# Kernel tuning notes

Hardware: AMD Instinct MI355X
Metric: run time of the kernel (lower is better)

Reference implementation:

```python
import jax, jax.numpy as jnp
import numpy as np

B, T, D = 64, 512, 1024
H0, H1 = 1024, 1024

def setup_inputs() -> dict:
    key = jax.random.key(0)
    k1, k2, k3 = jax.random.split(key, 3)
    # scale weights ~ 1/sqrt(fan_in) so tanh doesn't saturate
    s0 = 1.0 / np.sqrt(H0 + D)
    s1 = 1.0 / np.sqrt(H1 + H0)
    return {
        "x": jax.random.normal(k1, (B, T, D), dtype=jnp.float32),
        "W0": jax.random.normal(k2, (H0 + D, H0), dtype=jnp.float32) * s0,
        "b0": jnp.zeros((H0,), dtype=jnp.float32),
        "W1": jax.random.normal(k3, (H1 + H0, H1), dtype=jnp.float32) * s1,
        "b1": jnp.zeros((H1,), dtype=jnp.float32),
    }

def reference(x, W0, b0, W1, b1):
    batch = x.shape[0]
    h0_init = jnp.zeros((batch, W0.shape[1]), dtype=x.dtype)
    h1_init = jnp.zeros((batch, W1.shape[1]), dtype=x.dtype)

    def step(carry, xt):
        h0, h1 = carry
        # layer 0: concat(prev hidden, input) -> dense -> tanh
        h0 = jnp.tanh(jnp.concatenate([h0, xt], axis=-1) @ W0 + b0)
        # layer 1 consumes layer 0 output
        h1 = jnp.tanh(jnp.concatenate([h1, h0], axis=-1) @ W1 + b1)
        return (h0, h1), h1

    xs = jnp.swapaxes(x, 0, 1)  # [T, B, D] time-major for scan
    (h0_f, h1_f), ys = jax.lax.scan(step, (h0_init, h1_init), xs)
    outputs = jnp.swapaxes(ys, 0, 1)  # [B, T, H1]
    final_state = jnp.concatenate([h0_f, h1_f], axis=-1)  # [B, H0+H1]
    return outputs, final_state
```

## Files before the change

kernel.cpp:

```cpp
#include <hip/hip_runtime.h>
#include <cmath>


typedef unsigned short u16;
typedef unsigned int   u32;
typedef unsigned long long u64;
typedef __bf16 bf16x8 __attribute__((ext_vector_type(8)));
typedef u16    u16x8  __attribute__((ext_vector_type(8)));
typedef u16    u16x4  __attribute__((ext_vector_type(4)));
typedef float  f32x4  __attribute__((ext_vector_type(4)));

constexpr int BB = 64;
constexpr int TT = 512;
constexpr size_t SLOT   = (size_t)64 * 1024;
constexpr size_t SLAB_B = SLOT * 2;

constexpr size_t OFF_W0T = 262144;
constexpr size_t OFF_W1T = OFF_W0T + (size_t)1024 * 2048 * 2;
constexpr size_t OFF_R   = OFF_W1T + (size_t)1024 * 2048 * 2;

constexpr int LDS_REQ = 159744;

__device__ inline u16 f2bf(float f) { return __builtin_bit_cast(u16, (__bf16)f); }
__device__ inline float bf2f(u16 v) { return (float)__builtin_bit_cast(__bf16, v); }
__device__ inline float fast_tanh(float x) {
  x = fminf(15.f, fmaxf(-15.f, x));
  float e = __expf(2.f * x);
  return (e - 1.f) * __builtin_amdgcn_rcpf(e + 1.f);
}

__global__ void zero_flags(unsigned* f) {
  int i = blockIdx.x * 256 + threadIdx.x;
  if (i < 3 * 512 * 32) f[i] = 0;
}

__global__ void transpose_w(const float* __restrict__ W0,
                            const float* __restrict__ W1,
                            u16* __restrict__ wt_base) {
  __shared__ float tile[64][65];
  int bi  = blockIdx.x;
  int mat = bi >> 9;
  int t   = bi & 511;
  int tk = t & 31, tn = t >> 5;
  const float* W = mat ? W1 : W0;
  u16* Wt = wt_base + (size_t)mat * 1024 * 2048;
  int K0 = tk * 64, N0 = tn * 64;
  int tid = threadIdx.x;
  {
    int c4 = (tid & 15) * 4;
    int r  = tid >> 4;
    for (int i = 0; i < 4; ++i) {
      int kl = r + i * 16;
      float4 v = *(const float4*)(W + (size_t)(K0 + kl) * 1024 + N0 + c4);
      tile[kl][c4 + 0] = v.x; tile[kl][c4 + 1] = v.y;
      tile[kl][c4 + 2] = v.z; tile[kl][c4 + 3] = v.w;
    }
  }
  __syncthreads();
  {
    int nl = tid >> 3;
    int kc = (tid & 7) * 8;
    for (int pass = 0; pass < 2; ++pass) {
      int n = nl + pass * 32;
      u16x8 o;
      #pragma unroll
      for (int z = 0; z < 8; ++z) o[z] = f2bf(tile[kc + z][n]);
      *(u16x8*)(Wt + (size_t)(N0 + n) * 2048 + K0 + kc) = o;
    }
  }
}

__global__ void xconv(const float* __restrict__ x, u16* __restrict__ xb) {
  int bi = blockIdx.x;
  int b = bi >> 9, t = bi & 511;
  const float* src = x + ((size_t)b * TT + t) * 1024;
  u16* dst = xb + ((size_t)t * BB + b) * 1024;
  int i = threadIdx.x * 4;
  float4 v = *(const float4*)(src + i);
  u16x4 o; o[0] = f2bf(v.x); o[1] = f2bf(v.y); o[2] = f2bf(v.z); o[3] = f2bf(v.w);
  *(u16x4*)(dst + i) = o;
}

__device__ inline void poll1(unsigned* p) {
  while (__hip_atomic_load(p, __ATOMIC_RELAXED, __HIP_MEMORY_SCOPE_SYSTEM) == 0u)
    __builtin_amdgcn_s_sleep(1);
}

template<bool COHA>
__device__ inline void load_a8(const u16* Abase, size_t aoff, bf16x8* a) {
  const u16* ap = Abase + aoff;
  #pragma unroll
  for (int ks = 0; ks < 8; ++ks) {
    if constexpr (COHA) {
      u64 lo = __hip_atomic_load((u64*)(ap + ks * 32),     __ATOMIC_RELAXED, __HIP_MEMORY_SCOPE_SYSTEM);
      u64 hi = __hip_atomic_load((u64*)(ap + ks * 32 + 4), __ATOMIC_RELAXED, __HIP_MEMORY_SCOPE_SYSTEM);
      union { u64 q2[2]; bf16x8 v; } un; un.q2[0] = lo; un.q2[1] = hi;
      a[ks] = un.v;
    } else {
      a[ks] = __builtin_bit_cast(bf16x8, *(const u16x8*)(ap + ks * 32));
    }
  }
}

__device__ inline void fma8(const bf16x8* a, const u16* bp,
                            int gbase, int n15, f32x4& acc0, f32x4& acc1) {
  #pragma unroll
  for (int ks = 0; ks < 8; ++ks) {
    int g = (gbase + 4 * ks) ^ n15;
    bf16x8 b0 = __builtin_bit_cast(bf16x8, *(const u16x8*)(bp + g * 8));
    bf16x8 b1 = __builtin_bit_cast(bf16x8, *(const u16x8*)(bp + 16 * 1024 + g * 8));
    acc0 = __builtin_amdgcn_mfma_f32_16x16x32_bf16(a[ks], b0, acc0, 0, 0, 0);
    acc1 = __builtin_amdgcn_mfma_f32_16x16x32_bf16(a[ks], b1, acc1, 0, 0, 0);
  }
}

template<bool COH>
__global__ void __launch_bounds__(1024, 1)
rnn_seq(const float* __restrict__ x, const float* __restrict__ b0v,
        const float* __restrict__ b1v, float* __restrict__ out,
        unsigned* __restrict__ flags, const u16* __restrict__ W0t,
        const u16* __restrict__ W1t, u16* __restrict__ h0r,
        u16* __restrict__ h1r, u16* __restrict__ ur,
        const u16* __restrict__ xb, int use_xb) {
  constexpr int RMASK = COH ? 15 : 511;
  constexpr int UMASK = COH ? 31 : 511;
  constexpr int RING = 16, URING = 32;
  extern __shared__ u16 lds[];
  unsigned* fl_h0 = flags;
  unsigned* fl_h1 = flags + 512 * 32;
  unsigned* fl_u  = flags + 2 * 512 * 32;

  int wg = blockIdx.x, tid = threadIdx.x;
  int grp = wg >> 5, j = wg & 31;
  int n0 = j * 32;
  int lane = tid & 63, wave = tid >> 6;
  int rb = wave & 3;
  int ksl = wave >> 2;
  int n15 = lane & 15, q = lane >> 4;
  int r0 = rb * 16;

  u16*   wlds = lds;
  float* scr  = (float*)((char*)lds + ((grp == 1) ? 131072 : 65536));
  u16*   hch  = (u16*)((char*)scr + 24576);

  {
    const u16* Wt = (grp == 1) ? W1t : W0t;
    int nh = (grp == 1) ? 2 : 1;
    for (int h = 0; h < nh; ++h) {
      int kb = (grp == 1) ? h * 1024 : (grp == 2 ? 1024 : 0);
      for (int idx = tid; idx < 32 * 128; idx += 1024) {
        int n = idx >> 7, g = idx & 127;
        u16x8 v = *(const u16x8*)(Wt + (size_t)(n0 + n) * 2048 + kb + g * 8);
        *(u16x8*)(wlds + h * 32768 + n * 1024 + ((g ^ (n & 15)) * 8)) = v;
      }
    }
  }
  __syncthreads();

  const size_t aoff = (size_t)(r0 + n15) * 1024 + ksl * 256 + q * 8;
  const int gbase = 32 * ksl + q;
  const u16* bp0 = wlds + n15 * 1024;
  const u16* bp1 = wlds + 32768 + n15 * 1024;

  const int slice = wave >> 2;
  const int half  = slice >> 1;
  const int ksl2  = slice & 1;
  const size_t aoffS = (size_t)(r0 + n15) * 1024 + ksl2 * 512 + q * 8;
  const int gbaseS = 64 * ksl2 + q;
  const u16* bpH = half ? bp0 : bp1;

  const int sb  = tid >> 4;
  const int scc = (tid & 15) * 2;
  const int rbT = sb >> 4, rr = sb & 15;

  float bia = 0.f, bib = 0.f;
  if (grp == 1) { bia = b1v[n0 + n15]; bib = b1v[n0 + n15 + 16]; }
  float2 b2x = {0.f, 0.f};
  if (grp == 2) b2x = *(const float2*)&b0v[n0 + scc];

  auto scr_write = [&](int s, const f32x4& a0, const f32x4& a1) {
    int base = ((rb * 3 + s - 1) * 2) * 256 + (q * 4) * 16 + n15;
    #pragma unroll
    for (int i = 0; i < 4; ++i) scr[base + i * 16] = a0[i];
    #pragma unroll
    for (int i = 0; i < 4; ++i) scr[base + 256 + i * 16] = a1[i];
  };
  auto scr_sum = [&](f32x4& a0, f32x4& a1) {
    #pragma unroll
    for (int s = 0; s < 3; ++s) {
      int base = ((rb * 3 + s) * 2) * 256 + (q * 4) * 16 + n15;
      #pragma unroll
      for (int i = 0; i < 4; ++i) a0[i] += scr[base + i * 16];
      #pragma unroll
      for (int i = 0; i < 4; ++i) a1[i] += scr[base + 256 + i * 16];
    }
  };

  auto scr_put = [&](const f32x4& a0, const f32x4& a1) {
    int base = rb * 2048 + ksl * 512 + (q * 4) * 16 + n15;
    #pragma unroll
    for (int i = 0; i < 4; ++i) scr[base + i * 16] = a0[i];
    #pragma unroll
    for (int i = 0; i < 4; ++i) scr[base + 256 + i * 16] = a1[i];
  };
  auto col_sum = [&](int c2) -> float {
    int base = rbT * 2048 + (c2 >> 4) * 256 + rr * 16 + (c2 & 15);
    return (scr[base] + scr[base + 512]) + (scr[base + 1024] + scr[base + 1536]);
  };

  const size_t FIN = (size_t)BB * TT * 1024;

  if (grp == 0) {
    for (int t = 0; t < TT; ++t) {
      if (tid < 32)      { if (t > 0)            poll1(&fl_h0[(t - 1) * 32 + tid]); }
      else if (tid < 64) {                       poll1(&fl_u [t * 32 + (tid - 32)]); }
      else if (tid < 96) { if (COH && t >= RING) poll1(&fl_h1[(t - RING) * 32 + (tid - 64)]); }
      __syncthreads();
      bf16x8 a[8];
      if (t > 0) load_a8<COH>(h0r + (size_t)((t - 1) & RMASK) * SLOT, aoff, a);
      u32 uval;
      {
        const u32* up = (const u32*)(ur + (size_t)(t & UMASK) * SLOT + sb * 1024 + n0 + scc);
        uval = COH ? __hip_atomic_load((u32*)up, __ATOMIC_RELAXED, __HIP_MEMORY_SCOPE_SYSTEM)
                   : *up;
      }
      f32x4 acc0 = {0.f, 0.f, 0.f, 0.f}, acc1 = acc0;
      if (t > 0) fma8(a, bp0, gbase, n15, acc0, acc1);
      scr_put(acc0, acc1);
      __syncthreads();
      float v0 = fast_tanh(col_sum(scc)     + bf2f((u16)(uval & 0xffffu)));
      float v1 = fast_tanh(col_sum(scc + 1) + bf2f((u16)(uval >> 16)));
      u32 pv = (u32)f2bf(v0) | ((u32)f2bf(v1) << 16);
      __hip_atomic_store((u32*)(h0r + (size_t)(t & RMASK) * SLOT + sb * 1024 + n0 + scc),
                         pv, __ATOMIC_RELAXED, __HIP_MEMORY_SCOPE_SYSTEM);
      __syncthreads();
      if (tid == 0)
        __hip_atomic_store(&fl_h0[t * 32 + j], 1u, __ATOMIC_RELAXED, __HIP_MEMORY_SCOPE_SYSTEM);
      if (t == TT - 1) {
        float2 o; o.x = v0; o.y = v1;
        *(float2*)&out[FIN + (size_t)sb * 2048 + n0 + scc] = o;
      }
    }
  } else if (grp == 1) {
    for (int t = 0; t < TT; ++t) {
      if (tid < 32)      { poll1(&fl_h0[t * 32 + tid]); }
      else if (tid < 64) { if (t > 0) poll1(&fl_h1[(t - 1) * 32 + (tid - 32)]); }
      __syncthreads();
      f32x4 acc0 = {0.f, 0.f, 0.f, 0.f}, acc1 = acc0;
      if (half == 0) {
        bf16x8 a[16];
        const u16* s0 = h0r + (size_t)(t & RMASK) * SLOT;
        load_a8<COH>(s0, aoffS, a);
        load_a8<COH>(s0, aoffS + 256, a + 8);
        fma8(a,     bpH, gbaseS,      n15, acc0, acc1);
        fma8(a + 8, bpH, gbaseS + 32, n15, acc0, acc1);
      } else if (t > 0) {
        bf16x8 a[16];
        const u16* s1 = h1r + (size_t)((t - 1) & RMASK) * SLOT;
        load_a8<COH>(s1, aoffS, a);
        load_a8<COH>(s1, aoffS + 256, a + 8);
        fma8(a,     bpH, gbaseS,      n15, acc0, acc1);
        fma8(a + 8, bpH, gbaseS + 32, n15, acc0, acc1);
      }
      if (slice > 0) scr_write(slice, acc0, acc1);
      __syncthreads();
      if (slice == 0) {
        scr_sum(acc0, acc1);
        #pragma unroll
        for (int i = 0; i < 4; ++i) {
          int b = r0 + q * 4 + i;
          hch[b * 32 + n15]      = f2bf(fast_tanh(acc0[i] + bia));
          hch[b * 32 + n15 + 16] = f2bf(fast_tanh(acc1[i] + bib));
        }
      }
      __syncthreads();
      u32 pv = ((u32*)hch)[tid];
      __hip_atomic_store((u32*)(h1r + (size_t)(t & RMASK) * SLOT + sb * 1024 + n0 + scc),
                         pv, __ATOMIC_RELAXED, __HIP_MEMORY_SCOPE_SYSTEM);
      __syncthreads();
      if (tid == 0)
        __hip_atomic_store(&fl_h1[t * 32 + j], 1u, __ATOMIC_RELAXED, __HIP_MEMORY_SCOPE_SYSTEM);
      {
        float2 o; o.x = bf2f((u16)(pv & 0xffffu)); o.y = bf2f((u16)(pv >> 16));
        __builtin_nontemporal_store(o.x, &out[((size_t)sb * TT + t) * 1024 + n0 + scc]);
        __builtin_nontemporal_store(o.y, &out[((size_t)sb * TT + t) * 1024 + n0 + scc + 1]);
        if (t == TT - 1)
          *(float2*)&out[FIN + (size_t)sb * 2048 + 1024 + n0 + scc] = o;
      }
    }
  } else {
    for (int t = 0; t < TT; ++t) {
      if (COH && t >= URING) {
        if (tid < 32) poll1(&fl_h0[(t - URING) * 32 + tid]);
      }
      __syncthreads();
      bf16x8 a[8];
      if (use_xb) {
        load_a8<false>(xb + (size_t)t * SLOT, aoff, a);
      } else {
        const float* Ap = x + ((size_t)(r0 + n15) * TT + t) * 1024 + ksl * 256 + q * 8;
        float4 f[16];
        #pragma unroll
        for (int ks = 0; ks < 8; ++ks) {
          f[2 * ks]     = *(const float4*)(Ap + ks * 32);
          f[2 * ks + 1] = *(const float4*)(Ap + ks * 32 + 4);
        }
        #pragma unroll
        for (int ks = 0; ks < 8; ++ks) {
          bf16x8 tv;
          tv[0] = (__bf16)f[2*ks].x;   tv[1] = (__bf16)f[2*ks].y;
          tv[2] = (__bf16)f[2*ks].z;   tv[3] = (__bf16)f[2*ks].w;
          tv[4] = (__bf16)f[2*ks+1].x; tv[5] = (__bf16)f[2*ks+1].y;
          tv[6] = (__bf16)f[2*ks+1].z; tv[7] = (__bf16)f[2*ks+1].w;
          a[ks] = tv;
        }
      }
      f32x4 acc0 = {0.f, 0.f, 0.f, 0.f}, acc1 = acc0;
      fma8(a, bp0, gbase, n15, acc0, acc1);
      scr_put(acc0, acc1);
      __syncthreads();
      float v0 = col_sum(scc)     + b2x.x;
      float v1 = col_sum(scc + 1) + b2x.y;
      u32 pv = (u32)f2bf(v0) | ((u32)f2bf(v1) << 16);
      __hip_atomic_store((u32*)(ur + (size_t)(t & UMASK) * SLOT + sb * 1024 + n0 + scc),
                         pv, __ATOMIC_RELAXED, __HIP_MEMORY_SCOPE_SYSTEM);
      __syncthreads();
      if (tid == 0)
        __hip_atomic_store(&fl_u[t * 32 + j], 1u, __ATOMIC_RELAXED, __HIP_MEMORY_SCOPE_SYSTEM);
    }
  }
}

extern "C" void kernel_launch(void* const* d_in, const int* in_sizes, int n_in,
                              void* d_out, int out_size, void* d_ws, size_t ws_size,
                              hipStream_t stream) {
  const float* x  = (const float*)d_in[0];
  const float* W0 = (const float*)d_in[1];
  const float* b0 = (const float*)d_in[2];
  const float* W1 = (const float*)d_in[3];
  const float* b1 = (const float*)d_in[4];
  float* out = (float*)d_out;
  unsigned char* ws = (unsigned char*)d_ws;

  const size_t WS_PLAIN = OFF_R + 4ull * 512 * SLAB_B;
  bool plain = ws_size >= WS_PLAIN;
  size_t nslot  = plain ? 512 : 16;
  size_t nuslot = plain ? 512 : 32;
  size_t o_h0 = OFF_R;
  size_t o_h1 = o_h0 + nslot  * SLAB_B;
  size_t o_u  = o_h1 + nslot  * SLAB_B;
  size_t o_xb = o_u  + nuslot * SLAB_B;
  int use_xb = (plain || ws_size >= o_xb + (size_t)TT * SLAB_B) ? 1 : 0;

  unsigned* flags = (unsigned*)ws;
  const u16* W0t = (const u16*)(ws + OFF_W0T);
  const u16* W1t = (const u16*)(ws + OFF_W1T);
  u16* h0r = (u16*)(ws + o_h0);
  u16* h1r = (u16*)(ws + o_h1);
  u16* ur  = (u16*)(ws + o_u);
  u16* xb  = (u16*)(ws + o_xb);

  zero_flags<<<192, 256, 0, stream>>>(flags);
  transpose_w<<<1024, 256, 0, stream>>>(W0, W1, (u16*)(ws + OFF_W0T));
  if (use_xb) xconv<<<32768, 256, 0, stream>>>(x, xb);

  (void)hipFuncSetAttribute((const void*)rnn_seq<false>,
                            hipFuncAttributeMaxDynamicSharedMemorySize, LDS_REQ);
  (void)hipFuncSetAttribute((const void*)rnn_seq<true>,
                            hipFuncAttributeMaxDynamicSharedMemorySize, LDS_REQ);

  void* args[12];
  args[0]  = (void*)&x;    args[1]  = (void*)&b0;   args[2]  = (void*)&b1;
  args[3]  = (void*)&out;  args[4]  = (void*)&flags;
  args[5]  = (void*)&W0t;  args[6]  = (void*)&W1t;
  args[7]  = (void*)&h0r;  args[8]  = (void*)&h1r;  args[9]  = (void*)&ur;
  args[10] = (void*)&xb;   args[11] = (void*)&use_xb;
  hipLaunchCooperativeKernel(plain ? (void*)rnn_seq<false> : (void*)rnn_seq<true>,
                             dim3(96), dim3(1024), args, LDS_REQ, stream);
}
```

Before: 4.873 ms.

## Replace flag polling with sentinel-poisoned data polling in non-ring path

```diff
diff --git a/kernel.cpp b/kernel.cpp
--- a/kernel.cpp
+++ b/kernel.cpp
@@ -10,6 +10,9 @@
 typedef u16    u16x4  __attribute__((ext_vector_type(4)));
 typedef float  f32x4  __attribute__((ext_vector_type(4)));
 
+#define SCOPE_SYS __HIP_MEMORY_SCOPE_SYSTEM
+constexpr u32 SENT32 = 0x7FC07FC0u;
+
 constexpr int BB = 64;
 constexpr int TT = 512;
 constexpr size_t SLOT   = (size_t)64 * 1024;
@@ -32,6 +35,13 @@
 __global__ void zero_flags(unsigned* f) {
   int i = blockIdx.x * 256 + threadIdx.x;
   if (i < 3 * 512 * 32) f[i] = 0;
+}
+
+__global__ void poison(u32* p, size_t n4) {
+  size_t i = (size_t)blockIdx.x * 256 + threadIdx.x;
+  uint4 q = {SENT32, SENT32, SENT32, SENT32};
+  for (; i < n4; i += (size_t)gridDim.x * 256)
+    ((uint4*)p)[i] = q;
 }
 
 __global__ void transpose_w(const float* __restrict__ W0,
@@ -82,8 +92,39 @@
 }
 
 __device__ inline void poll1(unsigned* p) {
-  while (__hip_atomic_load(p, __ATOMIC_RELAXED, __HIP_MEMORY_SCOPE_SYSTEM) == 0u)
+  while (__hip_atomic_load(p, __ATOMIC_RELAXED, SCOPE_SYS) == 0u)
     __builtin_amdgcn_s_sleep(1);
+}
+
+template<int NF>
+__device__ inline void poll_frags(const u16* base, size_t off, bf16x8* a) {
+  const u16* p = base + off;
+  u64 lo[NF], hi[NF];
+  #pragma unroll
+  for (int i = 0; i < NF; ++i) {
+    lo[i] = __hip_atomic_load((const u64*)(p + i * 32),     __ATOMIC_RELAXED, SCOPE_SYS);
+    hi[i] = __hip_atomic_load((const u64*)(p + i * 32 + 4), __ATOMIC_RELAXED, SCOPE_SYS);
+  }
+  for (;;) {
+    u32 bad = 0;
+    #pragma unroll
+    for (int i = 0; i < NF; ++i) {
+      bad |= ((u32)lo[i] == SENT32) | ((u32)(lo[i] >> 32) == SENT32)
+           | ((u32)hi[i] == SENT32) | ((u32)(hi[i] >> 32) == SENT32);
+    }
+    if (!bad) break;
+    __builtin_amdgcn_s_sleep(1);
+    #pragma unroll
+    for (int i = 0; i < NF; ++i) {
+      lo[i] = __hip_atomic_load((const u64*)(p + i * 32),     __ATOMIC_RELAXED, SCOPE_SYS);
+      hi[i] = __hip_atomic_load((const u64*)(p + i * 32 + 4), __ATOMIC_RELAXED, SCOPE_SYS);
+    }
+  }
+  #pragma unroll
+  for (int i = 0; i < NF; ++i) {
+    union { u64 q2[2]; bf16x8 v; } un; un.q2[0] = lo[i]; un.q2[1] = hi[i];
+    a[i] = un.v;
+  }
 }
 
 template<bool COHA>
@@ -92,8 +133,8 @@
   #pragma unroll
   for (int ks = 0; ks < 8; ++ks) {
     if constexpr (COHA) {
-      u64 lo = __hip_atomic_load((u64*)(ap + ks * 32),     __ATOMIC_RELAXED, __HIP_MEMORY_SCOPE_SYSTEM);
-      u64 hi = __hip_atomic_load((u64*)(ap + ks * 32 + 4), __ATOMIC_RELAXED, __HIP_MEMORY_SCOPE_SYSTEM);
+      u64 lo = __hip_atomic_load((u64*)(ap + ks * 32),     __ATOMIC_RELAXED, SCOPE_SYS);
+      u64 hi = __hip_atomic_load((u64*)(ap + ks * 32 + 4), __ATOMIC_RELAXED, SCOPE_SYS);
       union { u64 q2[2]; bf16x8 v; } un; un.q2[0] = lo; un.q2[1] = hi;
       a[ks] = un.v;
     } else {
@@ -211,122 +252,226 @@
   const size_t FIN = (size_t)BB * TT * 1024;
 
   if (grp == 0) {
-    for (int t = 0; t < TT; ++t) {
-      if (tid < 32)      { if (t > 0)            poll1(&fl_h0[(t - 1) * 32 + tid]); }
-      else if (tid < 64) {                       poll1(&fl_u [t * 32 + (tid - 32)]); }
-      else if (tid < 96) { if (COH && t >= RING) poll1(&fl_h1[(t - RING) * 32 + (tid - 64)]); }
-      __syncthreads();
-      bf16x8 a[8];
-      if (t > 0) load_a8<COH>(h0r + (size_t)((t - 1) & RMASK) * SLOT, aoff, a);
-      u32 uval;
-      {
-        const u32* up = (const u32*)(ur + (size_t)(t & UMASK) * SLOT + sb * 1024 + n0 + scc);
-        uval = COH ? __hip_atomic_load((u32*)up, __ATOMIC_RELAXED, __HIP_MEMORY_SCOPE_SYSTEM)
-                   : *up;
-      }
-      f32x4 acc0 = {0.f, 0.f, 0.f, 0.f}, acc1 = acc0;
-      if (t > 0) fma8(a, bp0, gbase, n15, acc0, acc1);
-      scr_put(acc0, acc1);
-      __syncthreads();
-      float v0 = fast_tanh(col_sum(scc)     + bf2f((u16)(uval & 0xffffu)));
-      float v1 = fast_tanh(col_sum(scc + 1) + bf2f((u16)(uval >> 16)));
-      u32 pv = (u32)f2bf(v0) | ((u32)f2bf(v1) << 16);
-      __hip_atomic_store((u32*)(h0r + (size_t)(t & RMASK) * SLOT + sb * 1024 + n0 + scc),
-                         pv, __ATOMIC_RELAXED, __HIP_MEMORY_SCOPE_SYSTEM);
-      __syncthreads();
-      if (tid == 0)
-        __hip_atomic_store(&fl_h0[t * 32 + j], 1u, __ATOMIC_RELAXED, __HIP_MEMORY_SCOPE_SYSTEM);
-      if (t == TT - 1) {
-        float2 o; o.x = v0; o.y = v1;
-        *(float2*)&out[FIN + (size_t)sb * 2048 + n0 + scc] = o;
+    if constexpr (!COH) {
+      for (int t = 0; t < TT; ++t) {
+        const u32* up = (const u32*)(ur + (size_t)t * SLOT + sb * 1024 + n0 + scc);
+        u32 uval = __hip_atomic_load(up, __ATOMIC_RELAXED, SCOPE_SYS);
+        f32x4 acc0 = {0.f, 0.f, 0.f, 0.f}, acc1 = acc0;
+        if (t > 0) {
+          bf16x8 a[8];
+          poll_frags<8>(h0r + (size_t)(t - 1) * SLOT, aoff, a);
+          fma8(a, bp0, gbase, n15, acc0, acc1);
+        }
+        scr_put(acc0, acc1);
+        __syncthreads();
+        float s0 = col_sum(scc), s1 = col_sum(scc + 1);
+        while (uval == SENT32) {
+          __builtin_amdgcn_s_sleep(1);
+          uval = __hip_atomic_load(up, __ATOMIC_RELAXED, SCOPE_SYS);
+        }
+        float v0 = fast_tanh(s0 + bf2f((u16)(uval & 0xffffu)));
+        float v1 = fast_tanh(s1 + bf2f((u16)(uval >> 16)));
+        u32 pv = (u32)f2bf(v0) | ((u32)f2bf(v1) << 16);
+        __syncthreads();
+        __hip_atomic_store((u32*)(h0r + (size_t)t * SLOT + sb * 1024 + n0 + scc),
+                           pv, __ATOMIC_RELAXED, SCOPE_SYS);
+        if (t == TT - 1) {
+          float2 o; o.x = v0; o.y = v1;
+          *(float2*)&out[FIN + (size_t)sb * 2048 + n0 + scc] = o;
+        }
+      }
+    } else {
+      for (int t = 0; t < TT; ++t) {
+        if (tid < 32)      { if (t > 0)            poll1(&fl_h0[(t - 1) * 32 + tid]); }
+        else if (tid < 64) {                       poll1(&fl_u [t * 32 + (tid - 32)]); }
+        else if (tid < 96) { if (t >= RING)        poll1(&fl_h1[(t - RING) * 32 + (tid - 64)]); }
+        __syncthreads();
+        bf16x8 a[8];
+        if (t > 0) load_a8<true>(h0r + (size_t)((t - 1) & RMASK) * SLOT, aoff, a);
+        u32 uval;
+        {
+          const u32* up = (const u32*)(ur + (size_t)(t & UMASK) * SLOT + sb * 1024 + n0 + scc);
+          uval = __hip_atomic_load((u32*)up, __ATOMIC_RELAXED, SCOPE_SYS);
+        }
+        f32x4 acc0 = {0.f, 0.f, 0.f, 0.f}, acc1 = acc0;
+        if (t > 0) fma8(a, bp0, gbase, n15, acc0, acc1);
+        scr_put(acc0, acc1);
+        __syncthreads();
+        float v0 = fast_tanh(col_sum(scc)     + bf2f((u16)(uval & 0xffffu)));
+        float v1 = fast_tanh(col_sum(scc + 1) + bf2f((u16)(uval >> 16)));
+        u32 pv = (u32)f2bf(v0) | ((u32)f2bf(v1) << 16);
+        __hip_atomic_store((u32*)(h0r + (size_t)(t & RMASK) * SLOT + sb * 1024 + n0 + scc),
+                           pv, __ATOMIC_RELAXED, SCOPE_SYS);
+        __syncthreads();
+        if (tid == 0)
+          __hip_atomic_store(&fl_h0[t * 32 + j], 1u, __ATOMIC_RELAXED, SCOPE_SYS);
+        if (t == TT - 1) {
+          float2 o; o.x = v0; o.y = v1;
+          *(float2*)&out[FIN + (size_t)sb * 2048 + n0 + scc] = o;
+        }
       }
     }
   } else if (grp == 1) {
-    for (int t = 0; t < TT; ++t) {
-      if (tid < 32)      { poll1(&fl_h0[t * 32 + tid]); }
-      else if (tid < 64) { if (t > 0) poll1(&fl_h1[(t - 1) * 32 + (tid - 32)]); }
-      __syncthreads();
-      f32x4 acc0 = {0.f, 0.f, 0.f, 0.f}, acc1 = acc0;
-      if (half == 0) {
-        bf16x8 a[16];
-        const u16* s0 = h0r + (size_t)(t & RMASK) * SLOT;
-        load_a8<COH>(s0, aoffS, a);
-        load_a8<COH>(s0, aoffS + 256, a + 8);
-        fma8(a,     bpH, gbaseS,      n15, acc0, acc1);
-        fma8(a + 8, bpH, gbaseS + 32, n15, acc0, acc1);
-      } else if (t > 0) {
-        bf16x8 a[16];
-        const u16* s1 = h1r + (size_t)((t - 1) & RMASK) * SLOT;
-        load_a8<COH>(s1, aoffS, a);
-        load_a8<COH>(s1, aoffS + 256, a + 8);
-        fma8(a,     bpH, gbaseS,      n15, acc0, acc1);
-        fma8(a + 8, bpH, gbaseS + 32, n15, acc0, acc1);
-      }
-      if (slice > 0) scr_write(slice, acc0, acc1);
-      __syncthreads();
-      if (slice == 0) {
-        scr_sum(acc0, acc1);
-        #pragma unroll
-        for (int i = 0; i < 4; ++i) {
-          int b = r0 + q * 4 + i;
-          hch[b * 32 + n15]      = f2bf(fast_tanh(acc0[i] + bia));
-          hch[b * 32 + n15 + 16] = f2bf(fast_tanh(acc1[i] + bib));
-        }
-      }
-      __syncthreads();
-      u32 pv = ((u32*)hch)[tid];
-      __hip_atomic_store((u32*)(h1r + (size_t)(t & RMASK) * SLOT + sb * 1024 + n0 + scc),
-                         pv, __ATOMIC_RELAXED, __HIP_MEMORY_SCOPE_SYSTEM);
-      __syncthreads();
-      if (tid == 0)
-        __hip_atomic_store(&fl_h1[t * 32 + j], 1u, __ATOMIC_RELAXED, __HIP_MEMORY_SCOPE_SYSTEM);
-      {
-        float2 o; o.x = bf2f((u16)(pv & 0xffffu)); o.y = bf2f((u16)(pv >> 16));
-        __builtin_nontemporal_store(o.x, &out[((size_t)sb * TT + t) * 1024 + n0 + scc]);
-        __builtin_nontemporal_store(o.y, &out[((size_t)sb * TT + t) * 1024 + n0 + scc + 1]);
-        if (t == TT - 1)
-          *(float2*)&out[FIN + (size_t)sb * 2048 + 1024 + n0 + scc] = o;
+    if constexpr (!COH) {
+      for (int t = 0; t < TT; ++t) {
+        f32x4 acc0 = {0.f, 0.f, 0.f, 0.f}, acc1 = acc0;
+        if (half == 0) {
+          bf16x8 a[16];
+          poll_frags<16>(h0r + (size_t)t * SLOT, aoffS, a);
+          fma8(a,     bpH, gbaseS,      n15, acc0, acc1);
+          fma8(a + 8, bpH, gbaseS + 32, n15, acc0, acc1);
+        } else if (t > 0) {
+          bf16x8 a[16];
+          poll_frags<16>(h1r + (size_t)(t - 1) * SLOT, aoffS, a);
+          fma8(a,     bpH, gbaseS,      n15, acc0, acc1);
+          fma8(a + 8, bpH, gbaseS + 32, n15, acc0, acc1);
+        }
+        if (slice > 0) scr_write(slice, acc0, acc1);
+        __syncthreads();
+        if (slice == 0) {
+          scr_sum(acc0, acc1);
+          #pragma unroll
+          for (int i = 0; i < 4; ++i) {
+            int b = r0 + q * 4 + i;
+            hch[b * 32 + n15]      = f2bf(fast_tanh(acc0[i] + bia));
+            hch[b * 32 + n15 + 16] = f2bf(fast_tanh(acc1[i] + bib));
+          }
+        }
+        __syncthreads();
+        u32 pv = ((u32*)hch)[tid];
+        __hip_atomic_store((u32*)(h1r + (size_t)t * SLOT + sb * 1024 + n0 + scc),
+                           pv, __ATOMIC_RELAXED, SCOPE_SYS);
+        {
+          float2 o; o.x = bf2f((u16)(pv & 0xffffu)); o.y = bf2f((u16)(pv >> 16));
+          __builtin_nontemporal_store(o.x, &out[((size_t)sb * TT + t) * 1024 + n0 + scc]);
+          __builtin_nontemporal_store(o.y, &out[((size_t)sb * TT + t) * 1024 + n0 + scc + 1]);
+          if (t == TT - 1)
+            *(float2*)&out[FIN + (size_t)sb * 2048 + 1024 + n0 + scc] = o;
+        }
+      }
+    } else {
+      for (int t = 0; t < TT; ++t) {
+        if (tid < 32)      { poll1(&fl_h0[t * 32 + tid]); }
+        else if (tid < 64) { if (t > 0) poll1(&fl_h1[(t - 1) * 32 + (tid - 32)]); }
+        __syncthreads();
+        f32x4 acc0 = {0.f, 0.f, 0.f, 0.f}, acc1 = acc0;
+        if (half == 0) {
+          bf16x8 a[16];
+          const u16* s0 = h0r + (size_t)(t & RMASK) * SLOT;
+          load_a8<true>(s0, aoffS, a);
+          load_a8<true>(s0, aoffS + 256, a + 8);
+          fma8(a,     bpH, gbaseS,      n15, acc0, acc1);
+          fma8(a + 8, bpH, gbaseS + 32, n15, acc0, acc1);
+        } else if (t > 0) {
+          bf16x8 a[16];
+          const u16* s1 = h1r + (size_t)((t - 1) & RMASK) * SLOT;
+          load_a8<true>(s1, aoffS, a);
+          load_a8<true>(s1, aoffS + 256, a + 8);
+          fma8(a,     bpH, gbaseS,      n15, acc0, acc1);
+          fma8(a + 8, bpH, gbaseS + 32, n15, acc0, acc1);
+        }
+        if (slice > 0) scr_write(slice, acc0, acc1);
+        __syncthreads();
+        if (slice == 0) {
+          scr_sum(acc0, acc1);
+          #pragma unroll
+          for (int i = 0; i < 4; ++i) {
+            int b = r0 + q * 4 + i;
+            hch[b * 32 + n15]      = f2bf(fast_tanh(acc0[i] + bia));
+            hch[b * 32 + n15 + 16] = f2bf(fast_tanh(acc1[i] + bib));
+          }
+        }
+        __syncthreads();
+        u32 pv = ((u32*)hch)[tid];
+        __hip_atomic_store((u32*)(h1r + (size_t)(t & RMASK) * SLOT + sb * 1024 + n0 + scc),
+                           pv, __ATOMIC_RELAXED, SCOPE_SYS);
+        __syncthreads();
+        if (tid == 0)
+          __hip_atomic_store(&fl_h1[t * 32 + j], 1u, __ATOMIC_RELAXED, SCOPE_SYS);
+        {
+          float2 o; o.x = bf2f((u16)(pv & 0xffffu)); o.y = bf2f((u16)(pv >> 16));
+          __builtin_nontemporal_store(o.x, &out[((size_t)sb * TT + t) * 1024 + n0 + scc]);
+          __builtin_nontemporal_store(o.y, &out[((size_t)sb * TT + t) * 1024 + n0 + scc + 1]);
+          if (t == TT - 1)
+            *(float2*)&out[FIN + (size_t)sb * 2048 + 1024 + n0 + scc] = o;
+        }
       }
     }
   } else {
-    for (int t = 0; t < TT; ++t) {
-      if (COH && t >= URING) {
-        if (tid < 32) poll1(&fl_h0[(t - URING) * 32 + tid]);
-      }
-      __syncthreads();
-      bf16x8 a[8];
-      if (use_xb) {
-        load_a8<false>(xb + (size_t)t * SLOT, aoff, a);
-      } else {
-        const float* Ap = x + ((size_t)(r0 + n15) * TT + t) * 1024 + ksl * 256 + q * 8;
-        float4 f[16];
-        #pragma unroll
-        for (int ks = 0; ks < 8; ++ks) {
-          f[2 * ks]     = *(const float4*)(Ap + ks * 32);
-          f[2 * ks + 1] = *(const float4*)(Ap + ks * 32 + 4);
-        }
-        #pragma unroll
-        for (int ks = 0; ks < 8; ++ks) {
-          bf16x8 tv;
-          tv[0] = (__bf16)f[2*ks].x;   tv[1] = (__bf16)f[2*ks].y;
-          tv[2] = (__bf16)f[2*ks].z;   tv[3] = (__bf16)f[2*ks].w;
-          tv[4] = (__bf16)f[2*ks+1].x; tv[5] = (__bf16)f[2*ks+1].y;
-          tv[6] = (__bf16)f[2*ks+1].z; tv[7] = (__bf16)f[2*ks+1].w;
-          a[ks] = tv;
-        }
-      }
-      f32x4 acc0 = {0.f, 0.f, 0.f, 0.f}, acc1 = acc0;
-      fma8(a, bp0, gbase, n15, acc0, acc1);
-      scr_put(acc0, acc1);
-      __syncthreads();
-      float v0 = col_sum(scc)     + b2x.x;
-      float v1 = col_sum(scc + 1) + b2x.y;
-      u32 pv = (u32)f2bf(v0) | ((u32)f2bf(v1) << 16);
-      __hip_atomic_store((u32*)(ur + (size_t)(t & UMASK) * SLOT + sb * 1024 + n0 + scc),
-                         pv, __ATOMIC_RELAXED, __HIP_MEMORY_SCOPE_SYSTEM);
-      __syncthreads();
-      if (tid == 0)
-        __hip_atomic_store(&fl_u[t * 32 + j], 1u, __ATOMIC_RELAXED, __HIP_MEMORY_SCOPE_SYSTEM);
+    if constexpr (!COH) {
+      for (int t = 0; t < TT; ++t) {
+        bf16x8 a[8];
+        if (use_xb) {
+          load_a8<false>(xb + (size_t)t * SLOT, aoff, a);
+        } else {
+          const float* Ap = x + ((size_t)(r0 + n15) * TT + t) * 1024 + ksl * 256 + q * 8;
+          float4 f[16];
+          #pragma unroll
+          for (int ks = 0; ks < 8; ++ks) {
+            f[2 * ks]     = *(const float4*)(Ap + ks * 32);
+            f[2 * ks + 1] = *(const float4*)(Ap + ks * 32 + 4);
+          }
+          #pragma unroll
+          for (int ks = 0; ks < 8; ++ks) {
+            bf16x8 tv;
+            tv[0] = (__bf16)f[2*ks].x;   tv[1] = (__bf16)f[2*ks].y;
+            tv[2] = (__bf16)f[2*ks].z;   tv[3] = (__bf16)f[2*ks].w;
+            tv[4] = (__bf16)f[2*ks+1].x; tv[5] = (__bf16)f[2*ks+1].y;
+            tv[6] = (__bf16)f[2*ks+1].z; tv[7] = (__bf16)f[2*ks+1].w;
+            a[ks] = tv;
+          }
+        }
+        f32x4 acc0 = {0.f, 0.f, 0.f, 0.f}, acc1 = acc0;
+        fma8(a, bp0, gbase, n15, acc0, acc1);
+        scr_put(acc0, acc1);
+        __syncthreads();
+        float v0 = col_sum(scc)     + b2x.x;
+        float v1 = col_sum(scc + 1) + b2x.y;
+        u32 pv = (u32)f2bf(v0) | ((u32)f2bf(v1) << 16);
+        __syncthreads();
+        __hip_atomic_store((u32*)(ur + (size_t)t * SLOT + sb * 1024 + n0 + scc),
+                           pv, __ATOMIC_RELAXED, SCOPE_SYS);
+      }
+    } else {
+      for (int t = 0; t < TT; ++t) {
+        if (t >= URING) {
+          if (tid < 32) poll1(&fl_h0[(t - URING) * 32 + tid]);
+        }
+        __syncthreads();
+        bf16x8 a[8];
+        if (use_xb) {
+          load_a8<false>(xb + (size_t)t * SLOT, aoff, a);
+        } else {
+          const float* Ap = x + ((size_t)(r0 + n15) * TT + t) * 1024 + ksl * 256 + q * 8;
+          float4 f[16];
+          #pragma unroll
+          for (int ks = 0; ks < 8; ++ks) {
+            f[2 * ks]     = *(const float4*)(Ap + ks * 32);
+            f[2 * ks + 1] = *(const float4*)(Ap + ks * 32 + 4);
+          }
+          #pragma unroll
+          for (int ks = 0; ks < 8; ++ks) {
+            bf16x8 tv;
+            tv[0] = (__bf16)f[2*ks].x;   tv[1] = (__bf16)f[2*ks].y;
+            tv[2] = (__bf16)f[2*ks].z;   tv[3] = (__bf16)f[2*ks].w;
+            tv[4] = (__bf16)f[2*ks+1].x; tv[5] = (__bf16)f[2*ks+1].y;
+            tv[6] = (__bf16)f[2*ks+1].z; tv[7] = (__bf16)f[2*ks+1].w;
+            a[ks] = tv;
+          }
+        }
+        f32x4 acc0 = {0.f, 0.f, 0.f, 0.f}, acc1 = acc0;
+        fma8(a, bp0, gbase, n15, acc0, acc1);
+        scr_put(acc0, acc1);
+        __syncthreads();
+        float v0 = col_sum(scc)     + b2x.x;
+        float v1 = col_sum(scc + 1) + b2x.y;
+        u32 pv = (u32)f2bf(v0) | ((u32)f2bf(v1) << 16);
+        __hip_atomic_store((u32*)(ur + (size_t)(t & UMASK) * SLOT + sb * 1024 + n0 + scc),
+                           pv, __ATOMIC_RELAXED, SCOPE_SYS);
+        __syncthreads();
+        if (tid == 0)
+          __hip_atomic_store(&fl_u[t * 32 + j], 1u, __ATOMIC_RELAXED, SCOPE_SYS);
+      }
     }
   }
 }
@@ -363,6 +508,10 @@
   zero_flags<<<192, 256, 0, stream>>>(flags);
   transpose_w<<<1024, 256, 0, stream>>>(W0, W1, (u16*)(ws + OFF_W0T));
   if (use_xb) xconv<<<32768, 256, 0, stream>>>(x, xb);
+  if (plain) {
+    size_t n4 = (3ull * 512 * SLAB_B) / 16;
+    poison<<<4096, 256, 0, stream>>>((u32*)(ws + o_h0), n4);
+  }
 
   (void)hipFuncSetAttribute((const void*)rnn_seq<false>,
                             hipFuncAttributeMaxDynamicSharedMemorySize, LDS_REQ);
```

New measurement: 9.903 ms. 103% more time.
